# Kernel tuning notes

Measured on AMD Instinct MI355X. Metric: run time of the kernel, lower is better.

## Reference

```python
import jax, jax.numpy as jnp
import numpy as np

HIDDEN = 64

def setup_inputs() -> dict:
    key = jax.random.key(0)
    ks = jax.random.split(key, 6)
    inp = {
        "input_a": jax.random.normal(ks[0], (16, 6209, 256), dtype=jnp.float32),
        "input_b": jax.random.normal(ks[1], (16, 256, 256), dtype=jnp.float32),
        # Linear weights stored as [in, out]; xavier-ish scale
        "Wa": jax.random.normal(ks[2], (256, HIDDEN), dtype=jnp.float32) * (2.0 / (256 + HIDDEN)) ** 0.5,
        "ba": jnp.zeros((HIDDEN,), dtype=jnp.float32),
        "Wb": jax.random.normal(ks[3], (256, HIDDEN), dtype=jnp.float32) * (2.0 / (256 + HIDDEN)) ** 0.5,
        "bb": jnp.zeros((HIDDEN,), dtype=jnp.float32),
        "Wc": jax.random.normal(ks[4], (HIDDEN, 256), dtype=jnp.float32) * (2.0 / (HIDDEN + 256)) ** 0.5,
        "bc": jnp.zeros((256,), dtype=jnp.float32),
    }
    return inp

def reference(input_a, input_b, Wa, ba, Wb, bb, Wc, bc):
    # mapped_a: [b, dima, h], mapped_b: [b, dimb, h]
    mapped_a = jnp.einsum("bif,fh->bih", input_a, Wa) + ba
    mapped_b = jnp.einsum("bjf,fh->bjh", input_b, Wb) + bb
    # NOTE: original divides by scale = hidden**-0.5, i.e. multiplies by sqrt(hidden)
    scores = jnp.einsum("bih,bjh->bij", mapped_a, mapped_b) * jnp.sqrt(jnp.float32(HIDDEN))
    attn = jax.nn.softmax(scores, axis=-1)  # dropout is identity in eval
    out = jnp.einsum("bij,bjh->bih", attn, mapped_b)
    out = jnp.einsum("bih,hf->bif", out, Wc) + bc
    return out
```

## Files before the change

kernel.cpp:

```cpp
#include <hip/hip_runtime.h>

typedef float f32x4 __attribute__((ext_vector_type(4)));
typedef short s16x8 __attribute__((ext_vector_type(8)));

#define MFMA16(a, b, c) __builtin_amdgcn_mfma_f32_16x16x32_bf16((a), (b), (c), 0, 0, 0)

#define B_ 16
#define M_ 6209
#define F_ 256
#define NTR_ 389
#define NT_ 392

static __device__ __forceinline__ unsigned short f2bf(float x) {
    unsigned u = __builtin_bit_cast(unsigned, x);
    unsigned r = u + 0x7fffu + ((u >> 16) & 1u);
    return (unsigned short)(r >> 16);
}
static __device__ __forceinline__ float bf2f(unsigned short h) {
    unsigned u = ((unsigned)h) << 16;
    return __builtin_bit_cast(float, u);
}
static __device__ __forceinline__ void split_bf(float x, unsigned short& hi, unsigned short& lo) {
    hi = f2bf(x);
    lo = f2bf(x - bf2f(hi));
}
static __device__ __forceinline__ unsigned cvtpk_bf16(float a, float b) {
    unsigned r;
    asm("v_cvt_pk_bf16_f32 %0, %1, %2" : "=v"(r) : "v"(a), "v"(b));
    return r;
}

#define SW64(row, k)  ((row) * 64 + ((k) ^ (((row) & 7) << 3)))
#define SW256(row, k) ((row) * 256 + ((k) ^ (((row) & 7) << 3)))

__global__ __launch_bounds__(256) void k_prep(
    const float* __restrict__ inB, const float* __restrict__ Wb, const float* __restrict__ bb,
    const float* __restrict__ Wa, const float* __restrict__ Wc,
    float* __restrict__ mb,
    unsigned short* __restrict__ waf_hi, unsigned short* __restrict__ waf_lo,
    unsigned short* __restrict__ wcf) {
    const int blk = blockIdx.x;
    if (blk < 1024) {
        const int b = blk >> 6;
        const int j = (blk & 63) * 4 + (threadIdx.x >> 6);
        const int h = threadIdx.x & 63;
        const float* src = inB + ((size_t)(b * 256 + j)) * 256;
        float s = bb[h];
        #pragma unroll 4
        for (int f4 = 0; f4 < 64; ++f4) {
            const f32x4 v = *(const f32x4*)(src + f4 * 4);
            s = fmaf(v[0], Wb[(f4 * 4 + 0) * 64 + h], s);
            s = fmaf(v[1], Wb[(f4 * 4 + 1) * 64 + h], s);
            s = fmaf(v[2], Wb[(f4 * 4 + 2) * 64 + h], s);
            s = fmaf(v[3], Wb[(f4 * 4 + 3) * 64 + h], s);
        }
        mb[((size_t)(b * 256 + j)) * 64 + h] = s;
    } else {
        const int idx = (blk - 1024) * 256 + threadIdx.x;
        if (idx < 16384) {
            int i = idx;
            int jj = i & 7, lane = (i >> 3) & 63, nf = (i >> 9) & 3, ks = i >> 11;
            int g = lane >> 4, c = lane & 15;
            int f = ks * 32 + g * 8 + jj, h = nf * 16 + c;
            unsigned short hi, lo; split_bf(Wa[f * 64 + h], hi, lo);
            waf_hi[i] = hi; waf_lo[i] = lo;
        } else {
            int i = idx - 16384;
            int jj = i & 7, lane = (i >> 3) & 63, nf = (i >> 9) & 15, ks = i >> 13;
            int g = lane >> 4, c = lane & 15;
            int h = ks * 32 + g * 8 + jj, f = nf * 16 + c;
            wcf[i] = f2bf(Wc[h * 256 + f]);
        }
    }
}

__global__ __launch_bounds__(256, 3) void k_mapk(
    const float* __restrict__ A, const float* __restrict__ ba,
    const unsigned short* __restrict__ waf_hi, const unsigned short* __restrict__ waf_lo,
    const float* __restrict__ mb,
    unsigned short* __restrict__ mbb_hi, unsigned short* __restrict__ mbb_lo,
    unsigned short* __restrict__ mbp,
    unsigned short* __restrict__ mafh, unsigned short* __restrict__ mafl) {
    __shared__ __align__(16) unsigned short maH[4][2][1024];
    __shared__ __align__(16) unsigned short maL[4][2][1024];
    const int blk = blockIdx.x;
    if (blk < 784) {
        const int b = blk / 49, bx = blk % 49;
        const int w = threadIdx.x >> 6, lane = threadIdx.x & 63;
        const int g = lane >> 4, c = lane & 15;
        const int t0 = (bx * 4 + w) * 2;

        f32x4 accA[2][4];
        #pragma unroll
        for (int i = 0; i < 2; ++i)
            #pragma unroll
            for (int nf = 0; nf < 4; ++nf) { float v = ba[nf * 16 + c]; accA[i][nf] = (f32x4){v, v, v, v}; }
        const float* ab[2];
        #pragma unroll
        for (int i = 0; i < 2; ++i) {
            int arow = (t0 + i) * 16 + c; if (arow > M_ - 1) arow = M_ - 1;
            ab[i] = A + ((size_t)b * M_ + arow) * F_;
        }
        #pragma unroll
        for (int ks = 0; ks < 8; ++ks) {
            s16x8 ah[2], al[2];
            #pragma unroll
            for (int i = 0; i < 2; ++i) {
                const f32x4 a0 = *(const f32x4*)(ab[i] + ks * 32 + g * 8);
                const f32x4 a1 = *(const f32x4*)(ab[i] + ks * 32 + g * 8 + 4);
                #pragma unroll
                for (int j = 0; j < 4; ++j) {
                    unsigned short hi, lo;
                    split_bf(a0[j], hi, lo); ah[i][j] = (short)hi; al[i][j] = (short)lo;
                    split_bf(a1[j], hi, lo); ah[i][4 + j] = (short)hi; al[i][4 + j] = (short)lo;
                }
            }
            #pragma unroll
            for (int nf = 0; nf < 4; ++nf) {
                const int off = ((ks * 4 + nf) * 64 + lane) << 3;
                const s16x8 bh = *(const s16x8*)(waf_hi + off);
                const s16x8 bl = *(const s16x8*)(waf_lo + off);
                #pragma unroll
                for (int i = 0; i < 2; ++i) {
                    accA[i][nf] = MFMA16(ah[i], bh, accA[i][nf]);
                    accA[i][nf] = MFMA16(ah[i], bl, accA[i][nf]);
                    accA[i][nf] = MFMA16(al[i], bh, accA[i][nf]);
                }
            }
        }
        #pragma unroll
        for (int i = 0; i < 2; ++i)
            #pragma unroll
            for (int nf = 0; nf < 4; ++nf)
                #pragma unroll
                for (int r = 0; r < 4; ++r) {
                    unsigned short hi, lo; split_bf(accA[i][nf][r], hi, lo);
                    const int idx = SW64(g * 4 + r, nf * 16 + c);
                    maH[w][i][idx] = hi; maL[w][i][idx] = lo;
                }
        __syncthreads();
        #pragma unroll
        for (int i = 0; i < 2; ++i)
            #pragma unroll
            for (int ks = 0; ks < 2; ++ks) {
                const s16x8 fh = *(const s16x8*)&maH[w][i][SW64(c, ks * 32 + g * 8)];
                const s16x8 fl = *(const s16x8*)&maL[w][i][SW64(c, ks * 32 + g * 8)];
                const size_t off = (((size_t)(b * NT_ + t0 + i) * 2 + ks) * 64 + lane) << 3;
                *(s16x8*)(mafh + off) = fh;
                *(s16x8*)(mafl + off) = fl;
            }
    } else {
        const int i2 = (blk - 784) * 256 + threadIdx.x;
        if (i2 < 262144) {
            int i = i2;
            int jj = i & 7, lane = (i >> 3) & 63, nf = (i >> 9) & 15, ks = (i >> 13) & 1, b = i >> 14;
            int g = lane >> 4, c = lane & 15;
            int h = ks * 32 + g * 8 + jj, j = nf * 16 + c;
            unsigned short hi, lo; split_bf(mb[((size_t)(b * 256 + j)) * 64 + h], hi, lo);
            mbb_hi[i] = hi; mbb_lo[i] = lo;
        } else {
            int i = i2 - 262144;
            int jj = i & 7, lane = (i >> 3) & 63, nf = (i >> 9) & 3, ks = (i >> 11) & 7, b = i >> 14;
            int g = lane >> 4, c = lane & 15;
            int j = ks * 32 + g * 8 + jj, h = nf * 16 + c;
            mbp[i] = f2bf(mb[((size_t)(b * 256 + j)) * 64 + h]);
        }
    }
}

__global__ __launch_bounds__(256, 4) void k_attn2(
    const unsigned short* __restrict__ mafh, const unsigned short* __restrict__ mafl,
    const unsigned short* __restrict__ mbb_hi, const unsigned short* __restrict__ mbb_lo,
    const unsigned short* __restrict__ mbp, const unsigned short* __restrict__ wcf,
    const float* __restrict__ bc, float* __restrict__ out) {
    __shared__ __align__(16) unsigned short pSh[2][16 * 256];
    __shared__ __align__(16) unsigned short o1S[2][16 * 64];
    __shared__ float pmaxS[2][4][16];
    __shared__ float psumS[2][4][16];

    const int t0 = blockIdx.x * 2, b = blockIdx.y;
    const int w = threadIdx.x >> 6, lane = threadIdx.x & 63;
    const int g = lane >> 4, c = lane & 15;
    const float SC = 11.541560327f;

    s16x8 bh[2][2], bl[2][2];
    #pragma unroll
    for (int i = 0; i < 2; ++i)
        #pragma unroll
        for (int ks = 0; ks < 2; ++ks) {
            const size_t off = (((size_t)(b * NT_ + t0 + i) * 2 + ks) * 64 + lane) << 3;
            bh[i][ks] = *(const s16x8*)(mafh + off);
            bl[i][ks] = *(const s16x8*)(mafl + off);
        }

    f32x4 accST[2][4];
    #pragma unroll
    for (int i = 0; i < 2; ++i)
        #pragma unroll
        for (int jtl = 0; jtl < 4; ++jtl) accST[i][jtl] = (f32x4){0.f, 0.f, 0.f, 0.f};
    #pragma unroll
    for (int jtl = 0; jtl < 4; ++jtl) {
        const int jt = w * 4 + jtl;
        const size_t off0 = ((((size_t)b * 2 + 0) * 16 + jt) * 64 + lane) << 3;
        const size_t off1 = ((((size_t)b * 2 + 1) * 16 + jt) * 64 + lane) << 3;
        const s16x8 ah0 = *(const s16x8*)(mbb_hi + off0);
        const s16x8 al0 = *(const s16x8*)(mbb_lo + off0);
        const s16x8 ah1 = *(const s16x8*)(mbb_hi + off1);
        const s16x8 al1 = *(const s16x8*)(mbb_lo + off1);
        #pragma unroll
        for (int i = 0; i < 2; ++i) {
            f32x4 acc = accST[i][jtl];
            acc = MFMA16(ah0, bh[i][0], acc);
            acc = MFMA16(ah1, bh[i][1], acc);
            acc = MFMA16(ah0, bl[i][0], acc);
            acc = MFMA16(ah1, bl[i][1], acc);
            acc = MFMA16(al0, bh[i][0], acc);
            acc = MFMA16(al1, bh[i][1], acc);
            accST[i][jtl] = acc;
        }
    }

    #pragma unroll
    for (int i = 0; i < 2; ++i) {
        float m = accST[i][0][0];
        #pragma unroll
        for (int jtl = 0; jtl < 4; ++jtl) {
            m = fmaxf(m, accST[i][jtl][0]); m = fmaxf(m, accST[i][jtl][1]);
            m = fmaxf(m, accST[i][jtl][2]); m = fmaxf(m, accST[i][jtl][3]);
        }
        m = fmaxf(m, __shfl_xor(m, 16));
        m = fmaxf(m, __shfl_xor(m, 32));
        if (lane < 16) pmaxS[i][w][lane] = m;
    }
    __syncthreads();

    #pragma unroll
    for (int i = 0; i < 2; ++i) {
        const float mg = fmaxf(fmaxf(pmaxS[i][0][c], pmaxS[i][1][c]),
                               fmaxf(pmaxS[i][2][c], pmaxS[i][3][c]));
        float s = 0.f;
        #pragma unroll
        for (int jtl = 0; jtl < 4; ++jtl) {
            f32x4 p;
            #pragma unroll
            for (int r = 0; r < 4; ++r) {
                p[r] = __builtin_amdgcn_exp2f((accST[i][jtl][r] - mg) * SC);
                s += p[r];
            }
            const unsigned w0 = cvtpk_bf16(p[0], p[1]);
            const unsigned w1 = cvtpk_bf16(p[2], p[3]);
            const unsigned long long wv = (unsigned long long)w0 | ((unsigned long long)w1 << 32);
            *(unsigned long long*)&pSh[i][SW256(c, (w * 4 + jtl) * 16 + g * 4)] = wv;
        }
        s += __shfl_xor(s, 16);
        s += __shfl_xor(s, 32);
        if (lane < 16) psumS[i][w][lane] = s;
    }
    __syncthreads();

    f32x4 acc1[2] = {(f32x4){0.f, 0.f, 0.f, 0.f}, (f32x4){0.f, 0.f, 0.f, 0.f}};
    #pragma unroll
    for (int ks = 0; ks < 8; ++ks) {
        const size_t off = ((((size_t)b * 8 + ks) * 4 + w) * 64 + lane) << 3;
        const s16x8 av = *(const s16x8*)(mbp + off);
        #pragma unroll
        for (int i = 0; i < 2; ++i) {
            const s16x8 pf = *(const s16x8*)&pSh[i][SW256(c, ks * 32 + g * 8)];
            acc1[i] = MFMA16(av, pf, acc1[i]);
        }
    }
    #pragma unroll
    for (int i = 0; i < 2; ++i) {
        const float rinv = 1.f / (psumS[i][0][c] + psumS[i][1][c] + psumS[i][2][c] + psumS[i][3][c]);
        const unsigned w0 = cvtpk_bf16(acc1[i][0] * rinv, acc1[i][1] * rinv);
        const unsigned w1 = cvtpk_bf16(acc1[i][2] * rinv, acc1[i][3] * rinv);
        const unsigned long long wv = (unsigned long long)w0 | ((unsigned long long)w1 << 32);
        *(unsigned long long*)&o1S[i][SW64(c, w * 16 + g * 4)] = wv;
    }
    __syncthreads();

    s16x8 af[2][2];
    #pragma unroll
    for (int i = 0; i < 2; ++i)
        #pragma unroll
        for (int ks = 0; ks < 2; ++ks)
            af[i][ks] = *(const s16x8*)&o1S[i][SW64(c, ks * 32 + g * 8)];
    #pragma unroll
    for (int ftl = 0; ftl < 4; ++ftl) {
        const int ft = w * 4 + ftl;
        const float bv = bc[ft * 16 + c];
        const s16x8 wb0 = *(const s16x8*)(wcf + (((0 * 16 + ft) * 64 + lane) << 3));
        const s16x8 wb1 = *(const s16x8*)(wcf + (((1 * 16 + ft) * 64 + lane) << 3));
        #pragma unroll
        for (int i = 0; i < 2; ++i) {
            f32x4 acc = (f32x4){bv, bv, bv, bv};
            acc = MFMA16(af[i][0], wb0, acc);
            acc = MFMA16(af[i][1], wb1, acc);
            #pragma unroll
            for (int r = 0; r < 4; ++r) {
                const int q = (t0 + i) * 16 + g * 4 + r;
                if (q < M_) out[((size_t)b * M_ + q) * F_ + ft * 16 + c] = acc[r];
            }
        }
    }
}

extern "C" void kernel_launch(void* const* d_in, const int* in_sizes, int n_in,
                              void* d_out, int out_size, void* d_ws, size_t ws_size,
                              hipStream_t stream) {
    (void)in_sizes; (void)n_in; (void)out_size; (void)ws_size;
    const float* inA = (const float*)d_in[0];
    const float* inB = (const float*)d_in[1];
    const float* Wa  = (const float*)d_in[2];
    const float* ba  = (const float*)d_in[3];
    const float* Wb  = (const float*)d_in[4];
    const float* bb  = (const float*)d_in[5];
    const float* Wc  = (const float*)d_in[6];
    const float* bc  = (const float*)d_in[7];
    float* out = (float*)d_out;

    char* ws = (char*)d_ws;
    float* mb              = (float*)ws;
    unsigned short* waf_hi = (unsigned short*)(ws + 1048576);
    unsigned short* waf_lo = (unsigned short*)(ws + 1081344);
    unsigned short* wcf    = (unsigned short*)(ws + 1114112);
    unsigned short* mbb_hi = (unsigned short*)(ws + 1146880);
    unsigned short* mbb_lo = (unsigned short*)(ws + 1671168);
    unsigned short* mbp    = (unsigned short*)(ws + 2195456);
    unsigned short* mafh   = (unsigned short*)(ws + 2719744);
    unsigned short* mafl   = (unsigned short*)(ws + 15564800);

    hipLaunchKernelGGL(k_prep, dim3(1024 + 128), dim3(256), 0, stream,
                       inB, Wb, bb, Wa, Wc, mb, waf_hi, waf_lo, wcf);
    hipLaunchKernelGGL(k_mapk, dim3(784 + 2048), dim3(256), 0, stream,
                       inA, ba, waf_hi, waf_lo, mb, mbb_hi, mbb_lo, mbp, mafh, mafl);
    hipLaunchKernelGGL(k_attn2, dim3(195, B_), dim3(256), 0, stream,
                       mafh, mafl, mbb_hi, mbb_lo, mbp, wcf, bc, out);
}
```

Before: 81.88 us.

## Fuse A projection into attention kernel and write packed mapped_b in prep

The mapped_a projection now runs inside the attention kernel, with the hi/lo bf16 fragments kept in shared memory instead of written to and re-read from a ~25MB global workspace. The prep kernel writes mapped_b directly into the MFMA-packed hi/lo and transposed layouts, which removes the fp32 intermediate and the separate repack pass. This cuts the pipeline from three launches to two. In exchange, each attention block recomputes its own A tile with 4 waves over 32 rows, and the o1S buffer now aliases maH.

Result: slower. 91.33 us (+11.5%).

```diff
diff --git a/kernel.cpp b/kernel.cpp
--- a/kernel.cpp
+++ b/kernel.cpp
@@ -8,8 +8,6 @@
 #define B_ 16
 #define M_ 6209
 #define F_ 256
-#define NTR_ 389
-#define NT_ 392
 
 static __device__ __forceinline__ unsigned short f2bf(float x) {
     unsigned u = __builtin_bit_cast(unsigned, x);
@@ -36,9 +34,10 @@
 __global__ __launch_bounds__(256) void k_prep(
     const float* __restrict__ inB, const float* __restrict__ Wb, const float* __restrict__ bb,
     const float* __restrict__ Wa, const float* __restrict__ Wc,
-    float* __restrict__ mb,
     unsigned short* __restrict__ waf_hi, unsigned short* __restrict__ waf_lo,
-    unsigned short* __restrict__ wcf) {
+    unsigned short* __restrict__ wcf,
+    unsigned short* __restrict__ mbb_hi, unsigned short* __restrict__ mbb_lo,
+    unsigned short* __restrict__ mbp) {
     const int blk = blockIdx.x;
     if (blk < 1024) {
         const int b = blk >> 6;
@@ -54,7 +53,14 @@
             s = fmaf(v[2], Wb[(f4 * 4 + 2) * 64 + h], s);
             s = fmaf(v[3], Wb[(f4 * 4 + 3) * 64 + h], s);
         }
-        mb[((size_t)(b * 256 + j)) * 64 + h] = s;
+        unsigned short hi, lo; split_bf(s, hi, lo);
+        const int i1 = (b << 14) | ((h >> 5) << 13) | ((j >> 4) << 9)
+                     | (((h >> 3) & 3) << 7) | ((j & 15) << 3) | (h & 7);
+        mbb_hi[i1] = hi;
+        mbb_lo[i1] = lo;
+        const int i2 = (b << 14) | ((j >> 5) << 11) | ((h >> 4) << 9)
+                     | (((j >> 3) & 3) << 7) | ((h & 15) << 3) | (j & 7);
+        mbp[i2] = hi;
     } else {
         const int idx = (blk - 1024) * 256 + threadIdx.x;
         if (idx < 16384) {
@@ -74,123 +80,77 @@
     }
 }
 
-__global__ __launch_bounds__(256, 3) void k_mapk(
-    const float* __restrict__ A, const float* __restrict__ ba,
+__global__ __launch_bounds__(256, 4) void k_main(
+    const float* __restrict__ A, const float* __restrict__ ba, const float* __restrict__ bc,
     const unsigned short* __restrict__ waf_hi, const unsigned short* __restrict__ waf_lo,
-    const float* __restrict__ mb,
-    unsigned short* __restrict__ mbb_hi, unsigned short* __restrict__ mbb_lo,
-    unsigned short* __restrict__ mbp,
-    unsigned short* __restrict__ mafh, unsigned short* __restrict__ mafl) {
-    __shared__ __align__(16) unsigned short maH[4][2][1024];
-    __shared__ __align__(16) unsigned short maL[4][2][1024];
-    const int blk = blockIdx.x;
-    if (blk < 784) {
-        const int b = blk / 49, bx = blk % 49;
-        const int w = threadIdx.x >> 6, lane = threadIdx.x & 63;
-        const int g = lane >> 4, c = lane & 15;
-        const int t0 = (bx * 4 + w) * 2;
-
-        f32x4 accA[2][4];
-        #pragma unroll
-        for (int i = 0; i < 2; ++i)
-            #pragma unroll
-            for (int nf = 0; nf < 4; ++nf) { float v = ba[nf * 16 + c]; accA[i][nf] = (f32x4){v, v, v, v}; }
-        const float* ab[2];
-        #pragma unroll
-        for (int i = 0; i < 2; ++i) {
-            int arow = (t0 + i) * 16 + c; if (arow > M_ - 1) arow = M_ - 1;
-            ab[i] = A + ((size_t)b * M_ + arow) * F_;
-        }
-        #pragma unroll
-        for (int ks = 0; ks < 8; ++ks) {
-            s16x8 ah[2], al[2];
-            #pragma unroll
-            for (int i = 0; i < 2; ++i) {
-                const f32x4 a0 = *(const f32x4*)(ab[i] + ks * 32 + g * 8);
-                const f32x4 a1 = *(const f32x4*)(ab[i] + ks * 32 + g * 8 + 4);
-                #pragma unroll
-                for (int j = 0; j < 4; ++j) {
-                    unsigned short hi, lo;
-                    split_bf(a0[j], hi, lo); ah[i][j] = (short)hi; al[i][j] = (short)lo;
-                    split_bf(a1[j], hi, lo); ah[i][4 + j] = (short)hi; al[i][4 + j] = (short)lo;
-                }
-            }
-            #pragma unroll
-            for (int nf = 0; nf < 4; ++nf) {
-                const int off = ((ks * 4 + nf) * 64 + lane) << 3;
-                const s16x8 bh = *(const s16x8*)(waf_hi + off);
-                const s16x8 bl = *(const s16x8*)(waf_lo + off);
-                #pragma unroll
-                for (int i = 0; i < 2; ++i) {
-                    accA[i][nf] = MFMA16(ah[i], bh, accA[i][nf]);
-                    accA[i][nf] = MFMA16(ah[i], bl, accA[i][nf]);
-                    accA[i][nf] = MFMA16(al[i], bh, accA[i][nf]);
-                }
-            }
-        }
-        #pragma unroll
-        for (int i = 0; i < 2; ++i)
-            #pragma unroll
-            for (int nf = 0; nf < 4; ++nf)
-                #pragma unroll
-                for (int r = 0; r < 4; ++r) {
-                    unsigned short hi, lo; split_bf(accA[i][nf][r], hi, lo);
-                    const int idx = SW64(g * 4 + r, nf * 16 + c);
-                    maH[w][i][idx] = hi; maL[w][i][idx] = lo;
-                }
-        __syncthreads();
-        #pragma unroll
-        for (int i = 0; i < 2; ++i)
-            #pragma unroll
-            for (int ks = 0; ks < 2; ++ks) {
-                const s16x8 fh = *(const s16x8*)&maH[w][i][SW64(c, ks * 32 + g * 8)];
-                const s16x8 fl = *(const s16x8*)&maL[w][i][SW64(c, ks * 32 + g * 8)];
-                const size_t off = (((size_t)(b * NT_ + t0 + i) * 2 + ks) * 64 + lane) << 3;
-                *(s16x8*)(mafh + off) = fh;
-                *(s16x8*)(mafl + off) = fl;
-            }
-    } else {
-        const int i2 = (blk - 784) * 256 + threadIdx.x;
-        if (i2 < 262144) {
-            int i = i2;
-            int jj = i & 7, lane = (i >> 3) & 63, nf = (i >> 9) & 15, ks = (i >> 13) & 1, b = i >> 14;
-            int g = lane >> 4, c = lane & 15;
-            int h = ks * 32 + g * 8 + jj, j = nf * 16 + c;
-            unsigned short hi, lo; split_bf(mb[((size_t)(b * 256 + j)) * 64 + h], hi, lo);
-            mbb_hi[i] = hi; mbb_lo[i] = lo;
-        } else {
-            int i = i2 - 262144;
-            int jj = i & 7, lane = (i >> 3) & 63, nf = (i >> 9) & 3, ks = (i >> 11) & 7, b = i >> 14;
-            int g = lane >> 4, c = lane & 15;
-            int j = ks * 32 + g * 8 + jj, h = nf * 16 + c;
-            mbp[i] = f2bf(mb[((size_t)(b * 256 + j)) * 64 + h]);
-        }
-    }
-}
-
-__global__ __launch_bounds__(256, 4) void k_attn2(
-    const unsigned short* __restrict__ mafh, const unsigned short* __restrict__ mafl,
+    const unsigned short* __restrict__ wcf,
     const unsigned short* __restrict__ mbb_hi, const unsigned short* __restrict__ mbb_lo,
-    const unsigned short* __restrict__ mbp, const unsigned short* __restrict__ wcf,
-    const float* __restrict__ bc, float* __restrict__ out) {
+    const unsigned short* __restrict__ mbp,
+    float* __restrict__ out) {
+    __shared__ __align__(16) unsigned short maH[2][1024];
+    __shared__ __align__(16) unsigned short maL[2][1024];
     __shared__ __align__(16) unsigned short pSh[2][16 * 256];
-    __shared__ __align__(16) unsigned short o1S[2][16 * 64];
     __shared__ float pmaxS[2][4][16];
     __shared__ float psumS[2][4][16];
+    unsigned short* o1S = &maH[0][0];
 
     const int t0 = blockIdx.x * 2, b = blockIdx.y;
     const int w = threadIdx.x >> 6, lane = threadIdx.x & 63;
     const int g = lane >> 4, c = lane & 15;
     const float SC = 11.541560327f;
 
+    {
+        const int i0 = w >> 1, hh = w & 1;
+        f32x4 accA[2];
+        #pragma unroll
+        for (int nf2 = 0; nf2 < 2; ++nf2) {
+            float v = ba[(hh * 2 + nf2) * 16 + c];
+            accA[nf2] = (f32x4){v, v, v, v};
+        }
+        int arow = (t0 + i0) * 16 + c; if (arow > M_ - 1) arow = M_ - 1;
+        const float* abase = A + ((size_t)b * M_ + arow) * F_;
+        #pragma unroll
+        for (int ks = 0; ks < 8; ++ks) {
+            const f32x4 a0 = *(const f32x4*)(abase + ks * 32 + g * 8);
+            const f32x4 a1 = *(const f32x4*)(abase + ks * 32 + g * 8 + 4);
+            s16x8 ah, al;
+            #pragma unroll
+            for (int j = 0; j < 4; ++j) {
+                unsigned short hi, lo;
+                split_bf(a0[j], hi, lo); ah[j] = (short)hi; al[j] = (short)lo;
+                split_bf(a1[j], hi, lo); ah[4 + j] = (short)hi; al[4 + j] = (short)lo;
+            }
+            #pragma unroll
+            for (int nf2 = 0; nf2 < 2; ++nf2) {
+                const int nf = hh * 2 + nf2;
+                const int off = ((ks * 4 + nf) * 64 + lane) << 3;
+                const s16x8 bh = *(const s16x8*)(waf_hi + off);
+                const s16x8 bl = *(const s16x8*)(waf_lo + off);
+                accA[nf2] = MFMA16(ah, bh, accA[nf2]);
+                accA[nf2] = MFMA16(ah, bl, accA[nf2]);
+                accA[nf2] = MFMA16(al, bh, accA[nf2]);
+            }
+        }
+        #pragma unroll
+        for (int nf2 = 0; nf2 < 2; ++nf2) {
+            const int nf = hh * 2 + nf2;
+            #pragma unroll
+            for (int r = 0; r < 4; ++r) {
+                unsigned short hi, lo; split_bf(accA[nf2][r], hi, lo);
+                const int idx = SW64(g * 4 + r, nf * 16 + c);
+                maH[i0][idx] = hi; maL[i0][idx] = lo;
+            }
+        }
+    }
+    __syncthreads();
+
     s16x8 bh[2][2], bl[2][2];
     #pragma unroll
     for (int i = 0; i < 2; ++i)
         #pragma unroll
         for (int ks = 0; ks < 2; ++ks) {
-            const size_t off = (((size_t)(b * NT_ + t0 + i) * 2 + ks) * 64 + lane) << 3;
-            bh[i][ks] = *(const s16x8*)(mafh + off);
-            bl[i][ks] = *(const s16x8*)(mafl + off);
+            bh[i][ks] = *(const s16x8*)&maH[i][SW64(c, ks * 32 + g * 8)];
+            bl[i][ks] = *(const s16x8*)&maL[i][SW64(c, ks * 32 + g * 8)];
         }
 
     f32x4 accST[2][4];
@@ -275,7 +235,7 @@
         const unsigned w0 = cvtpk_bf16(acc1[i][0] * rinv, acc1[i][1] * rinv);
         const unsigned w1 = cvtpk_bf16(acc1[i][2] * rinv, acc1[i][3] * rinv);
         const unsigned long long wv = (unsigned long long)w0 | ((unsigned long long)w1 << 32);
-        *(unsigned long long*)&o1S[i][SW64(c, w * 16 + g * 4)] = wv;
+        *(unsigned long long*)&o1S[i * 1024 + SW64(c, w * 16 + g * 4)] = wv;
     }
     __syncthreads();
 
@@ -284,7 +244,7 @@
     for (int i = 0; i < 2; ++i)
         #pragma unroll
         for (int ks = 0; ks < 2; ++ks)
-            af[i][ks] = *(const s16x8*)&o1S[i][SW64(c, ks * 32 + g * 8)];
+            af[i][ks] = *(const s16x8*)&o1S[i * 1024 + SW64(c, ks * 32 + g * 8)];
     #pragma unroll
     for (int ftl = 0; ftl < 4; ++ftl) {
         const int ft = w * 4 + ftl;
@@ -320,20 +280,15 @@
     float* out = (float*)d_out;
 
     char* ws = (char*)d_ws;
-    float* mb              = (float*)ws;
-    unsigned short* waf_hi = (unsigned short*)(ws + 1048576);
-    unsigned short* waf_lo = (unsigned short*)(ws + 1081344);
-    unsigned short* wcf    = (unsigned short*)(ws + 1114112);
-    unsigned short* mbb_hi = (unsigned short*)(ws + 1146880);
-    unsigned short* mbb_lo = (unsigned short*)(ws + 1671168);
-    unsigned short* mbp    = (unsigned short*)(ws + 2195456);
-    unsigned short* mafh   = (unsigned short*)(ws + 2719744);
-    unsigned short* mafl   = (unsigned short*)(ws + 15564800);
+    unsigned short* waf_hi = (unsigned short*)ws;
+    unsigned short* waf_lo = (unsigned short*)(ws + 32768);
+    unsigned short* wcf    = (unsigned short*)(ws + 65536);
+    unsigned short* mbb_hi = (unsigned short*)(ws + 98304);
+    unsigned short* mbb_lo = (unsigned short*)(ws + 622592);
+    unsigned short* mbp    = (unsigned short*)(ws + 1146880);
 
     hipLaunchKernelGGL(k_prep, dim3(1024 + 128), dim3(256), 0, stream,
-                       inB, Wb, bb, Wa, Wc, mb, waf_hi, waf_lo, wcf);
-    hipLaunchKernelGGL(k_mapk, dim3(784 + 2048), dim3(256), 0, stream,
-                       inA, ba, waf_hi, waf_lo, mb, mbb_hi, mbb_lo, mbp, mafh, mafl);
-    hipLaunchKernelGGL(k_attn2, dim3(195, B_), dim3(256), 0, stream,
-                       mafh, mafl, mbb_hi, mbb_lo, mbp, wcf, bc, out);
-}
+                       inB, Wb, bb, Wa, Wc, waf_hi, waf_lo, wcf, mbb_hi, mbb_lo, mbp);
+    hipLaunchKernelGGL(k_main, dim3(195, B_), dim3(256), 0, stream,
+                       inA, ba, bc, waf_hi, waf_lo, wcf, mbb_hi, mbb_lo, mbp, out);
+}
```
